# Kernel tuning notes

Measured on AMD Instinct MI355X. Metric: run time of the kernel, lower is better.

## Reference

```python
import jax, jax.numpy as jnp
import numpy as np

ALPHA = 1.0  # module hardcodes self.alpha = 1.0


def _normalize(m):
    # torch: diag(rowsum^-0.5) @ m @ diag(rowsum^-0.5) == broadcast row/col scaling
    r_inv = jnp.sum(m, axis=0) ** -0.5  # [V]
    return m * r_inv[:, None] * r_inv[None, :]


def setup_inputs() -> dict:
    key = jax.random.key(0)
    k1, k2, k3, k4 = jax.random.split(key, 4)
    V, D_IN, D_OUT, A, B = 2048, 64, 64, 8, 8
    adj = jax.random.uniform(k1, (V, V), dtype=jnp.float32)
    x = jax.random.normal(k2, (A, B, V, D_IN), dtype=jnp.float32)
    # xavier_normal_ on [D_IN, D_OUT]
    std = float(np.sqrt(2.0 / (D_IN + D_OUT)))
    weight = jax.random.normal(k3, (D_IN, D_OUT), dtype=jnp.float32) * std
    bias = jax.random.normal(k4, (D_OUT,), dtype=jnp.float32)
    return {"adj": adj, "x": x, "weight": weight, "bias": bias}


def reference(adj, x, weight, bias):
    # dropout is identity in eval mode
    adj_norm = _normalize(adj)
    sqr_norm = _normalize(adj @ adj)  # computed as in the original (alpha=1 zeroes it)
    m_norm = ALPHA * adj_norm + (1.0 - ALPHA) * sqr_norm  # [V, V]
    x_tmp = jnp.einsum('abvd,de->abve', x, weight)        # project features
    x_out = jnp.einsum('vj,abvd->abjd', m_norm, x_tmp)    # aggregate over nodes
    x_out = x_out + bias
    return jax.nn.relu(x_out)
```

## Files before the change

kernel.cpp:

```cpp
#include <hip/hip_runtime.h>
#include <cstddef>

typedef unsigned short u16;
typedef u16 u16x8 __attribute__((ext_vector_type(8)));
typedef __bf16 bf16x8 __attribute__((ext_vector_type(8)));
typedef float f32x4 __attribute__((ext_vector_type(4)));

static constexpr int V  = 2048;
static constexpr int DD = 64;

__device__ __forceinline__ u16 f2b(float f) {
  union { float f; unsigned int i; } x; x.f = f;
  return (u16)((x.i + 0x7fffu + ((x.i >> 16) & 1u)) >> 16);
}

__device__ __forceinline__ void gll16(const void* g, void* l) {
  __builtin_amdgcn_global_load_lds(
      (const __attribute__((address_space(1))) void*)g,
      (__attribute__((address_space(3))) void*)l, 16, 0, 0);
}

__global__ __launch_bounds__(256) void k_part(const float* __restrict__ adj,
                                              float* __restrict__ partial) {
  int t = threadIdx.x;
  int r0 = blockIdx.x * 32;
  int c0 = t * 8;
  float acc[8] = {0.f, 0.f, 0.f, 0.f, 0.f, 0.f, 0.f, 0.f};
  for (int r = 0; r < 32; ++r) {
    const float4* p = (const float4*)(adj + (size_t)(r0 + r) * V + c0);
    float4 a0 = p[0], a1 = p[1];
    acc[0] += a0.x; acc[1] += a0.y; acc[2] += a0.z; acc[3] += a0.w;
    acc[4] += a1.x; acc[5] += a1.y; acc[6] += a1.z; acc[7] += a1.w;
  }
  #pragma unroll
  for (int k = 0; k < 8; ++k) partial[(size_t)blockIdx.x * V + c0 + k] = acc[k];
}

__global__ __launch_bounds__(256) void k_prep(const float* __restrict__ adj,
                                              const float* __restrict__ partial,
                                              const float* __restrict__ x,
                                              const float* __restrict__ w,
                                              u16* __restrict__ At,
                                              u16* __restrict__ Yt) {
  __shared__ float T[64][65];
  __shared__ float rvv[64], rvj[64];
  int t = threadIdx.x;
  int bid = blockIdx.x;

  if (bid < 1024) {
    int v0 = (bid & 31) * 64;
    int j0 = (bid >> 5) * 64;
    if (t < 128) {
      int col = (t < 64) ? (v0 + t) : (j0 + (t - 64));
      float s = 0.f;
      for (int i = 0; i < 64; ++i) s += partial[(size_t)i * V + col];
      float rv = rsqrtf(s);
      if (t < 64) rvv[t] = rv; else rvj[t - 64] = rv;
    }
    __syncthreads();
    #pragma unroll
    for (int it = 0; it < 2; ++it) {
      int f = t + it * 256;
      int row = f >> 3;
      int cc = (f & 7) * 8;
      float rv = rvv[row];
      const float4* p = (const float4*)(adj + (size_t)(v0 + row) * V + j0 + cc);
      float4 a0 = p[0], a1 = p[1];
      T[row][cc + 0] = a0.x * rv; T[row][cc + 1] = a0.y * rv;
      T[row][cc + 2] = a0.z * rv; T[row][cc + 3] = a0.w * rv;
      T[row][cc + 4] = a1.x * rv; T[row][cc + 5] = a1.y * rv;
      T[row][cc + 6] = a1.z * rv; T[row][cc + 7] = a1.w * rv;
    }
    __syncthreads();
    #pragma unroll
    for (int it = 0; it < 2; ++it) {
      int f = t + it * 256;
      int jr = f >> 3;
      int vc = (f & 7) * 8;
      float rj = rvj[jr];
      u16x8 o;
      #pragma unroll
      for (int k = 0; k < 8; ++k) o[k] = f2b(T[vc + k][jr] * rj);
      *(u16x8*)(At + (size_t)(j0 + jr) * V + v0 + vc) = o;
    }
  } else {
    int pb = bid - 1024;
    int ab = pb >> 4;
    int v0 = (pb & 15) * 128;
    u16* WT = (u16*)&T[0][0];

    {
      const float4* pw = (const float4*)(w + t * 16);
      float4 c0 = pw[0], c1 = pw[1], c2 = pw[2], c3 = pw[3];
      float vals[16] = {c0.x, c0.y, c0.z, c0.w, c1.x, c1.y, c1.z, c1.w,
                        c2.x, c2.y, c2.z, c2.w, c3.x, c3.y, c3.z, c3.w};
      #pragma unroll
      for (int k = 0; k < 16; ++k) {
        int idx = t * 16 + k;
        WT[(idx & 63) * 72 + (idx >> 6)] = f2b(vals[k]);
      }
    }
    __syncthreads();

    int lane = t & 63, wave = t >> 6;
    int q = lane >> 4, r = lane & 15;
    int vbase = v0 + wave * 32;

    bf16x8 a[4][2];
    #pragma unroll
    for (int i = 0; i < 4; ++i)
      #pragma unroll
      for (int kk = 0; kk < 2; ++kk)
        a[i][kk] = __builtin_bit_cast(bf16x8,
            *(const u16x8*)(WT + (i * 16 + r) * 72 + kk * 32 + q * 8));

    const f32x4 vzero = {0.f, 0.f, 0.f, 0.f};
    f32x4 acc[4][2];
    #pragma unroll
    for (int i = 0; i < 4; ++i) { acc[i][0] = vzero; acc[i][1] = vzero; }

    #pragma unroll
    for (int nt = 0; nt < 2; ++nt) {
      int v = vbase + nt * 16 + r;
      const float* xp = x + ((size_t)ab * V + v) * DD;
      #pragma unroll
      for (int kk = 0; kk < 2; ++kk) {
        const float4* p = (const float4*)(xp + kk * 32 + q * 8);
        float4 b0 = p[0], b1 = p[1];
        u16x8 bu;
        bu[0] = f2b(b0.x); bu[1] = f2b(b0.y); bu[2] = f2b(b0.z); bu[3] = f2b(b0.w);
        bu[4] = f2b(b1.x); bu[5] = f2b(b1.y); bu[6] = f2b(b1.z); bu[7] = f2b(b1.w);
        bf16x8 bf = __builtin_bit_cast(bf16x8, bu);
        #pragma unroll
        for (int i = 0; i < 4; ++i)
          acc[i][nt] = __builtin_amdgcn_mfma_f32_16x16x32_bf16(a[i][kk], bf, acc[i][nt], 0, 0, 0);
      }
    }

    #pragma unroll
    for (int i = 0; i < 4; ++i)
      #pragma unroll
      for (int nt = 0; nt < 2; ++nt) {
        int v = vbase + nt * 16 + r;
        #pragma unroll
        for (int reg = 0; reg < 4; ++reg) {
          int e = i * 16 + q * 4 + reg;
          Yt[(size_t)(ab * 64 + e) * V + v] = f2b(acc[i][nt][reg]);
        }
      }
  }
}

#define BM 128
#define BN 128
#define PANEL (128 * 32)

__global__ __launch_bounds__(256) void k_gemm(const u16* __restrict__ At,
                                              const u16* __restrict__ Yt,
                                              const float* __restrict__ bias,
                                              float* __restrict__ out) {
  __shared__ u16 Al[4 * PANEL];
  __shared__ u16 Bl[4 * PANEL];
  int t = threadIdx.x;
  int m0 = blockIdx.x * BM;
  int n0 = blockIdx.y * BN;
  int lane = t & 63;
  int wave = t >> 6;
  int wm = (wave & 1) * 64;
  int wn = (wave >> 1) * 64;
  int q = lane >> 4;
  int r = lane & 15;

  const f32x4 vzero = {0.f, 0.f, 0.f, 0.f};
  f32x4 acc[4][4];
  #pragma unroll
  for (int i = 0; i < 4; ++i)
    #pragma unroll
    for (int j = 0; j < 4; ++j) acc[i][j] = vzero;

  int eo0 = t * 8;
  int eo1 = (256 + t) * 8;
  int row0 = eo0 >> 5, col0 = eo0 & 31;
  int row1 = eo1 >> 5, col1 = eo1 & 31;

  for (int k0 = 0; k0 < V; k0 += 128) {
    __syncthreads();
    #pragma unroll
    for (int p = 0; p < 4; ++p) {
      int kp = k0 + p * 32;
      gll16(At + (size_t)(m0 + row0) * V + kp + col0, Al + p * PANEL + eo0);
      gll16(At + (size_t)(m0 + row1) * V + kp + col1, Al + p * PANEL + eo1);
      gll16(Yt + (size_t)(n0 + row0) * V + kp + col0, Bl + p * PANEL + eo0);
      gll16(Yt + (size_t)(n0 + row1) * V + kp + col1, Bl + p * PANEL + eo1);
    }
    __syncthreads();
    #pragma unroll
    for (int p = 0; p < 4; ++p) {
      bf16x8 a[4], b[4];
      #pragma unroll
      for (int i = 0; i < 4; ++i)
        a[i] = __builtin_bit_cast(bf16x8,
            *(const u16x8*)(Al + p * PANEL + (wm + i * 16 + r) * 32 + q * 8));
      #pragma unroll
      for (int j = 0; j < 4; ++j)
        b[j] = __builtin_bit_cast(bf16x8,
            *(const u16x8*)(Bl + p * PANEL + (wn + j * 16 + r) * 32 + q * 8));
      #pragma unroll
      for (int i = 0; i < 4; ++i)
        #pragma unroll
        for (int j = 0; j < 4; ++j)
          acc[i][j] = __builtin_amdgcn_mfma_f32_16x16x32_bf16(a[i], b[j], acc[i][j], 0, 0, 0);
    }
  }

  #pragma unroll
  for (int j = 0; j < 4; ++j) {
    int n = n0 + wn + j * 16 + r;
    int e = n & 63;
    int ab = n >> 6;
    float bv = bias[e];
    float* ob = out + (size_t)ab * (V * DD);
    #pragma unroll
    for (int i = 0; i < 4; ++i) {
      #pragma unroll
      for (int reg = 0; reg < 4; ++reg) {
        int jj = m0 + wm + i * 16 + q * 4 + reg;
        ob[(size_t)jj * DD + e] = fmaxf(acc[i][j][reg] + bv, 0.f);
      }
    }
  }
}

extern "C" void kernel_launch(void* const* d_in, const int* in_sizes, int n_in,
                              void* d_out, int out_size, void* d_ws, size_t ws_size,
                              hipStream_t stream) {
  const float* adj  = (const float*)d_in[0];
  const float* x    = (const float*)d_in[1];
  const float* w    = (const float*)d_in[2];
  const float* bias = (const float*)d_in[3];
  float* out = (float*)d_out;

  char* ws = (char*)d_ws;
  u16*   At      = (u16*)ws;
  u16*   Yt      = (u16*)(ws + ((size_t)8 << 20));
  float* partial = (float*)(ws + ((size_t)24 << 20));

  k_part<<<64, 256, 0, stream>>>(adj, partial);
  k_prep<<<2048, 256, 0, stream>>>(adj, partial, x, w, At, Yt);
  k_gemm<<<dim3(16, 32), 256, 0, stream>>>(At, Yt, bias, out);
}
```

Measured before the change: 150.3 us.

## Triple-buffer GEMM LDS with swizzled layout, 128x256 tiles and 8 waves

The main GEMM is rebuilt as a software pipeline. Global-to-LDS loads are issued two K-steps ahead into a three-slot ring buffer, with vmcnt waits and per-phase barriers, instead of loading then synchronising every 128-wide K chunk. The LDS layout is XOR-swizzled to avoid bank conflicts. Tiles grow to 128x256 with 512 threads, and s_setprio is raised around the MFMA bursts. This aims to hide load latency and cut redundant tile reloads, but adds more barriers and a fragile hand-tuned waitcnt schedule.

```diff
diff --git a/kernel.cpp b/kernel.cpp
--- a/kernel.cpp
+++ b/kernel.cpp
@@ -151,25 +151,33 @@
   }
 }
 
-#define BM 128
-#define BN 128
-#define PANEL (128 * 32)
-
-__global__ __launch_bounds__(256) void k_gemm(const u16* __restrict__ At,
+static constexpr int BUF_U16 = 24576;
+
+__global__ __launch_bounds__(512) void k_gemm(const u16* __restrict__ At,
                                               const u16* __restrict__ Yt,
                                               const float* __restrict__ bias,
                                               float* __restrict__ out) {
-  __shared__ u16 Al[4 * PANEL];
-  __shared__ u16 Bl[4 * PANEL];
-  int t = threadIdx.x;
-  int m0 = blockIdx.x * BM;
-  int n0 = blockIdx.y * BN;
-  int lane = t & 63;
-  int wave = t >> 6;
-  int wm = (wave & 1) * 64;
-  int wn = (wave >> 1) * 64;
-  int q = lane >> 4;
-  int r = lane & 15;
+  __shared__ u16 lds[3 * BUF_U16];
+  const int t = threadIdx.x;
+  const int m0 = blockIdx.x * 128;
+  const int n0 = blockIdx.y * 256;
+  const int lane = t & 63, wave = t >> 6;
+  const int wm = (wave & 1) * 64;
+  const int wn = (wave >> 1) * 64;
+  const int q = lane >> 4, r = lane & 15;
+
+  auto stA = [&](int sb, int k0, int l) {
+    int g = l * 512 + t;
+    int row = g >> 3;
+    int ch = (((g & 7) ^ (row & 7)) << 3);
+    gll16(At + (size_t)(m0 + row) * V + k0 + ch, (void*)(lds + sb + g * 8));
+  };
+  auto stB = [&](int sb, int k0, int l) {
+    int g = l * 512 + t;
+    int row = g >> 3;
+    int ch = (((g & 7) ^ (row & 7)) << 3);
+    gll16(Yt + (size_t)(n0 + row) * V + k0 + ch, (void*)(lds + sb + 8192 + g * 8));
+  };
 
   const f32x4 vzero = {0.f, 0.f, 0.f, 0.f};
   f32x4 acc[4][4];
@@ -178,38 +186,68 @@
     #pragma unroll
     for (int j = 0; j < 4; ++j) acc[i][j] = vzero;
 
-  int eo0 = t * 8;
-  int eo1 = (256 + t) * 8;
-  int row0 = eo0 >> 5, col0 = eo0 & 31;
-  int row1 = eo1 >> 5, col1 = eo1 & 31;
-
-  for (int k0 = 0; k0 < V; k0 += 128) {
-    __syncthreads();
+  stA(0, 0, 0); stA(0, 0, 1);
+  stB(0, 0, 0); stB(0, 0, 1); stB(0, 0, 2); stB(0, 0, 3);
+  stA(BUF_U16, 64, 0); stA(BUF_U16, 64, 1);
+  stB(BUF_U16, 64, 0); stB(BUF_U16, 64, 1); stB(BUF_U16, 64, 2); stB(BUF_U16, 64, 3);
+  asm volatile("s_waitcnt vmcnt(6)" ::: "memory");
+  __builtin_amdgcn_s_barrier();
+
+  for (int tt = 0; tt < 32; ++tt) {
+    const int cbase = (tt % 3) * BUF_U16;
+    const int sbase = ((tt + 2) % 3) * BUF_U16;
+    const int sk0 = (tt + 2) * 64;
+    const bool st = (tt < 30);
+
     #pragma unroll
     for (int p = 0; p < 4; ++p) {
-      int kp = k0 + p * 32;
-      gll16(At + (size_t)(m0 + row0) * V + kp + col0, Al + p * PANEL + eo0);
-      gll16(At + (size_t)(m0 + row1) * V + kp + col1, Al + p * PANEL + eo1);
-      gll16(Yt + (size_t)(n0 + row0) * V + kp + col0, Bl + p * PANEL + eo0);
-      gll16(Yt + (size_t)(n0 + row1) * V + kp + col1, Bl + p * PANEL + eo1);
-    }
-    __syncthreads();
-    #pragma unroll
-    for (int p = 0; p < 4; ++p) {
-      bf16x8 a[4], b[4];
-      #pragma unroll
-      for (int i = 0; i < 4; ++i)
-        a[i] = __builtin_bit_cast(bf16x8,
-            *(const u16x8*)(Al + p * PANEL + (wm + i * 16 + r) * 32 + q * 8));
-      #pragma unroll
-      for (int j = 0; j < 4; ++j)
-        b[j] = __builtin_bit_cast(bf16x8,
-            *(const u16x8*)(Bl + p * PANEL + (wn + j * 16 + r) * 32 + q * 8));
-      #pragma unroll
-      for (int i = 0; i < 4; ++i)
-        #pragma unroll
-        for (int j = 0; j < 4; ++j)
-          acc[i][j] = __builtin_amdgcn_mfma_f32_16x16x32_bf16(a[i], b[j], acc[i][j], 0, 0, 0);
+      const int ip = (p & 1) * 2;
+      const int jp = (p >> 1) * 2;
+
+      bf16x8 aq[2][2], bq[2][2];
+      #pragma unroll
+      for (int ii = 0; ii < 2; ++ii) {
+        const int row = wm + (ip + ii) * 16 + r;
+        #pragma unroll
+        for (int kk = 0; kk < 2; ++kk)
+          aq[ii][kk] = __builtin_bit_cast(bf16x8,
+              *(const u16x8*)(lds + cbase + row * 64 +
+                              (((kk * 4 + q) ^ (row & 7)) << 3)));
+      }
+      #pragma unroll
+      for (int jj = 0; jj < 2; ++jj) {
+        const int row = wn + (jp + jj) * 16 + r;
+        #pragma unroll
+        for (int kk = 0; kk < 2; ++kk)
+          bq[jj][kk] = __builtin_bit_cast(bf16x8,
+              *(const u16x8*)(lds + cbase + 8192 + row * 64 +
+                              (((kk * 4 + q) ^ (row & 7)) << 3)));
+      }
+
+      if (st) {
+        if (p == 0)      { stA(sbase, sk0, 0); stA(sbase, sk0, 1); }
+        else if (p == 1) { stB(sbase, sk0, 0); stB(sbase, sk0, 1); }
+        else if (p == 2) { stB(sbase, sk0, 2); stB(sbase, sk0, 3); }
+      }
+
+      __builtin_amdgcn_s_barrier();
+      asm volatile("s_waitcnt lgkmcnt(0)" ::: "memory");
+      __builtin_amdgcn_s_setprio(1);
+      #pragma unroll
+      for (int kk = 0; kk < 2; ++kk)
+        #pragma unroll
+        for (int ii = 0; ii < 2; ++ii)
+          #pragma unroll
+          for (int jj = 0; jj < 2; ++jj)
+            acc[ip + ii][jp + jj] = __builtin_amdgcn_mfma_f32_16x16x32_bf16(
+                aq[ii][kk], bq[jj][kk], acc[ip + ii][jp + jj], 0, 0, 0);
+      __builtin_amdgcn_s_setprio(0);
+
+      if (p == 3) {
+        if (tt < 30)       asm volatile("s_waitcnt vmcnt(6)" ::: "memory");
+        else if (tt == 30) asm volatile("s_waitcnt vmcnt(0)" ::: "memory");
+      }
+      __builtin_amdgcn_s_barrier();
     }
   }
 
@@ -247,5 +285,5 @@
 
   k_part<<<64, 256, 0, stream>>>(adj, partial);
   k_prep<<<2048, 256, 0, stream>>>(adj, partial, x, w, At, Yt);
-  k_gemm<<<dim3(16, 32), 256, 0, stream>>>(At, Yt, bias, out);
-}
+  k_gemm<<<dim3(16, 16), 512, 0, stream>>>(At, Yt, bias, out);
+}
```

After: 154.4 us. 2.7% more time.

## Double-buffer GEMM LDS tiles with XOR swizzle and larger 128x256 block tile

Applied to the files above, without the earlier changes.

Rewrites the main GEMM as a double-buffered pipeline. The next K-slice of 64 is prefetched via global_load_lds while MFMAs run on the current buffer, which replaces the previous load-then-compute loop. The block tile grows from 128x128 to 128x256, so each wave computes 128x64 with 32 accumulators. An XOR swizzle is added on LDS chunks to avoid bank conflicts, a block-index remap is added for L2 locality, and setprio is raised around the MFMA bursts. Register pressure rises, and the grid drops to 256 blocks, which may underfill the CUs.

```diff
diff --git a/kernel.cpp b/kernel.cpp
--- a/kernel.cpp
+++ b/kernel.cpp
@@ -151,66 +151,88 @@
   }
 }
 
-#define BM 128
-#define BN 128
-#define PANEL (128 * 32)
+static constexpr int ABUF  = 128 * 64;
+static constexpr int BBUF  = 256 * 64;
+static constexpr int BUFSZ = ABUF + BBUF;
 
 __global__ __launch_bounds__(256) void k_gemm(const u16* __restrict__ At,
                                               const u16* __restrict__ Yt,
                                               const float* __restrict__ bias,
                                               float* __restrict__ out) {
-  __shared__ u16 Al[4 * PANEL];
-  __shared__ u16 Bl[4 * PANEL];
-  int t = threadIdx.x;
-  int m0 = blockIdx.x * BM;
-  int n0 = blockIdx.y * BN;
-  int lane = t & 63;
-  int wave = t >> 6;
-  int wm = (wave & 1) * 64;
-  int wn = (wave >> 1) * 64;
-  int q = lane >> 4;
-  int r = lane & 15;
+  __shared__ u16 lds[2 * BUFSZ];
+  const int t = threadIdx.x;
+  const int bid = blockIdx.x;
+  const int swz = (bid & 7) * 32 + (bid >> 3);
+  const int m0 = (swz & 15) * 128;
+  const int n0 = (swz >> 4) * 256;
+  const int lane = t & 63, wave = t >> 6;
+  const int wn = wave * 64;
+  const int q = lane >> 4, r = lane & 15;
+
+  auto stage = [&](int base, int k0) {
+    #pragma unroll
+    for (int l = 0; l < 4; ++l) {
+      int g = l * 256 + t;
+      int row = g >> 3, cl = g & 7;
+      int ch = cl ^ (row & 7);
+      gll16(At + (size_t)(m0 + row) * V + k0 + ch * 8, (void*)(lds + base + g * 8));
+    }
+    #pragma unroll
+    for (int l = 0; l < 8; ++l) {
+      int g = l * 256 + t;
+      int row = g >> 3, cl = g & 7;
+      int ch = cl ^ (row & 7);
+      gll16(Yt + (size_t)(n0 + row) * V + k0 + ch * 8, (void*)(lds + base + ABUF + g * 8));
+    }
+  };
 
   const f32x4 vzero = {0.f, 0.f, 0.f, 0.f};
-  f32x4 acc[4][4];
+  f32x4 acc[8][4];
   #pragma unroll
-  for (int i = 0; i < 4; ++i)
+  for (int i = 0; i < 8; ++i)
     #pragma unroll
     for (int j = 0; j < 4; ++j) acc[i][j] = vzero;
 
-  int eo0 = t * 8;
-  int eo1 = (256 + t) * 8;
-  int row0 = eo0 >> 5, col0 = eo0 & 31;
-  int row1 = eo1 >> 5, col1 = eo1 & 31;
-
-  for (int k0 = 0; k0 < V; k0 += 128) {
-    __syncthreads();
-    #pragma unroll
-    for (int p = 0; p < 4; ++p) {
-      int kp = k0 + p * 32;
-      gll16(At + (size_t)(m0 + row0) * V + kp + col0, Al + p * PANEL + eo0);
-      gll16(At + (size_t)(m0 + row1) * V + kp + col1, Al + p * PANEL + eo1);
-      gll16(Yt + (size_t)(n0 + row0) * V + kp + col0, Bl + p * PANEL + eo0);
-      gll16(Yt + (size_t)(n0 + row1) * V + kp + col1, Bl + p * PANEL + eo1);
-    }
-    __syncthreads();
-    #pragma unroll
-    for (int p = 0; p < 4; ++p) {
-      bf16x8 a[4], b[4];
-      #pragma unroll
-      for (int i = 0; i < 4; ++i)
+  stage(0, 0);
+  asm volatile("s_waitcnt vmcnt(0)" ::: "memory");
+  __builtin_amdgcn_s_barrier();
+
+  int cb = 0;
+  for (int tt = 0; tt < 32; ++tt) {
+    const int nb = cb ^ BUFSZ;
+    if (tt < 31) stage(nb, (tt + 1) * 64);
+    __builtin_amdgcn_sched_barrier(0);
+
+    #pragma unroll
+    for (int kk = 0; kk < 2; ++kk) {
+      bf16x8 a[8], b[4];
+      #pragma unroll
+      for (int i = 0; i < 8; ++i) {
+        int row = i * 16 + r;
+        int c = (kk * 4 + q) ^ (row & 7);
         a[i] = __builtin_bit_cast(bf16x8,
-            *(const u16x8*)(Al + p * PANEL + (wm + i * 16 + r) * 32 + q * 8));
-      #pragma unroll
-      for (int j = 0; j < 4; ++j)
+            *(const u16x8*)(lds + cb + row * 64 + c * 8));
+      }
+      #pragma unroll
+      for (int j = 0; j < 4; ++j) {
+        int row = wn + j * 16 + r;
+        int c = (kk * 4 + q) ^ (row & 7);
         b[j] = __builtin_bit_cast(bf16x8,
-            *(const u16x8*)(Bl + p * PANEL + (wn + j * 16 + r) * 32 + q * 8));
-      #pragma unroll
-      for (int i = 0; i < 4; ++i)
+            *(const u16x8*)(lds + cb + ABUF + row * 64 + c * 8));
+      }
+      __builtin_amdgcn_s_setprio(1);
+      #pragma unroll
+      for (int i = 0; i < 8; ++i)
         #pragma unroll
         for (int j = 0; j < 4; ++j)
-          acc[i][j] = __builtin_amdgcn_mfma_f32_16x16x32_bf16(a[i], b[j], acc[i][j], 0, 0, 0);
-    }
+          acc[i][j] = __builtin_amdgcn_mfma_f32_16x16x32_bf16(
+              a[i], b[j], acc[i][j], 0, 0, 0);
+      __builtin_amdgcn_s_setprio(0);
+    }
+
+    asm volatile("s_waitcnt vmcnt(0)" ::: "memory");
+    __builtin_amdgcn_s_barrier();
+    cb = nb;
   }
 
   #pragma unroll
@@ -221,10 +243,10 @@
     float bv = bias[e];
     float* ob = out + (size_t)ab * (V * DD);
     #pragma unroll
-    for (int i = 0; i < 4; ++i) {
+    for (int i = 0; i < 8; ++i) {
       #pragma unroll
       for (int reg = 0; reg < 4; ++reg) {
-        int jj = m0 + wm + i * 16 + q * 4 + reg;
+        int jj = m0 + i * 16 + q * 4 + reg;
         ob[(size_t)jj * DD + e] = fmaxf(acc[i][j][reg] + bv, 0.f);
       }
     }
@@ -247,5 +269,5 @@
 
   k_part<<<64, 256, 0, stream>>>(adj, partial);
   k_prep<<<2048, 256, 0, stream>>>(adj, partial, x, w, At, Yt);
-  k_gemm<<<dim3(16, 32), 256, 0, stream>>>(At, Yt, bias, out);
-}
+  k_gemm<<<256, 256, 0, stream>>>(At, Yt, bias, out);
+}
```

After: 161.2 us. 7.2% more time.
